# Kernel tuning notes

Hardware: AMD Instinct MI355X
Metric: run time of the kernel (lower is better)

## Reference

```python
import jax, jax.numpy as jnp
import numpy as np

N = 100000
E = 1600000
IN_FEATS = 256
HID = 128


def _graph_conv(x, W, b, src, dst, n_nodes):
    # DGL GraphConv with norm='both':
    #   out = D_in^{-1/2} * A * (D_out^{-1/2} * x @ W) + b
    ones = jnp.ones(src.shape[0], dtype=x.dtype)
    deg_out = jax.ops.segment_sum(ones, src, num_segments=n_nodes)
    deg_in = jax.ops.segment_sum(ones, dst, num_segments=n_nodes)
    norm_src = jnp.maximum(deg_out, 1.0) ** -0.5  # [N]
    norm_dst = jnp.maximum(deg_in, 1.0) ** -0.5   # [N]
    h = (x * norm_src[:, None]) @ W               # [N, HID]
    msg = h[src]                                  # [E, HID] gather
    agg = jax.ops.segment_sum(msg, dst, num_segments=n_nodes)  # [N, HID] scatter-add
    return agg * norm_dst[:, None] + b


def setup_inputs() -> dict:
    key = jax.random.key(0)
    ks = jax.random.split(key, 12)
    x = jax.random.normal(ks[0], (N, IN_FEATS), dtype=jnp.float32)
    src0 = jax.random.randint(ks[1], (E,), 0, N, dtype=jnp.int32)
    dst0 = jax.random.randint(ks[2], (E,), 0, N, dtype=jnp.int32)
    src1 = jax.random.randint(ks[3], (E,), 0, N, dtype=jnp.int32)
    dst1 = jax.random.randint(ks[4], (E,), 0, N, dtype=jnp.int32)
    s_e = 1.0 / np.sqrt(IN_FEATS)
    s_h = 1.0 / np.sqrt(HID)
    We = jax.random.uniform(ks[5], (IN_FEATS, HID), jnp.float32, -s_e, s_e)
    be = jax.random.uniform(ks[6], (HID,), jnp.float32, -s_e, s_e)
    W1 = jax.random.uniform(ks[7], (HID, HID), jnp.float32, -s_h, s_h)
    b1 = jnp.zeros((HID,), jnp.float32)
    W2 = jax.random.uniform(ks[8], (HID, HID), jnp.float32, -s_h, s_h)
    b2 = jnp.zeros((HID,), jnp.float32)
    return {"x": x, "We": We, "be": be, "W1": W1, "b1": b1, "W2": W2, "b2": b2,
            "src0": src0, "dst0": dst0, "src1": src1, "dst1": dst1}


def reference(x, We, be, W1, b1, W2, b2, src0, dst0, src1, dst1):
    n = x.shape[0]
    h = x @ We + be                                   # embed
    h = jax.nn.relu(_graph_conv(h, W1, b1, src0, dst0, n))
    h = jax.nn.relu(_graph_conv(h, W2, b2, src1, dst1, n))
    return h
```

## Files before the change

kernel.cpp:

```cpp
#include <hip/hip_runtime.h>

#define HID 128
#define NBUCK 512
#define BSHIFT 8
#define NB 512
#define M4 (4 * NBUCK * NB)
#define STAGE_CAP 8192
#define PCAP 7168

typedef __attribute__((ext_vector_type(8))) short bf16x8;
typedef __attribute__((ext_vector_type(4))) float f32x4;

__device__ __forceinline__ unsigned short f2bf(float f) {
    union { float f; unsigned u; } v; v.f = f;
    unsigned r = v.u + 0x7fff + ((v.u >> 16) & 1);
    return (unsigned short)(r >> 16);
}
__device__ __forceinline__ float bf2f(unsigned short b) {
    union { float f; unsigned u; } v; v.u = ((unsigned)b) << 16;
    return v.f;
}

__device__ __forceinline__ void gload_lds16(const void* g, void* l) {
    __builtin_amdgcn_global_load_lds(
        (const __attribute__((address_space(1))) void*)g,
        (__attribute__((address_space(3))) void*)l, 16, 0, 0);
}

__global__ __launch_bounds__(256) void bucket_count_all(
    const int* __restrict__ k0, const int* __restrict__ k1,
    const int* __restrict__ k2, const int* __restrict__ k3,
    int* __restrict__ counts, int E, int chunk) {
    __shared__ int h[4][NBUCK];
    int tid = threadIdx.x;
    #pragma unroll
    for (int j = 0; j < 8; ++j) ((int*)h)[tid + j * 256] = 0;
    __syncthreads();
    int base = blockIdx.x * chunk;
    int end = min(base + chunk, E);
    const int* keys[4] = {k0, k1, k2, k3};
    #pragma unroll
    for (int p = 0; p < 4; ++p) {
        const int* kp = keys[p];
        for (int i = base + tid; i < end; i += 256)
            atomicAdd(&h[p][kp[i] >> BSHIFT], 1);
    }
    __syncthreads();
    #pragma unroll
    for (int p = 0; p < 4; ++p) {
        counts[((p << 9) + tid) * NB + blockIdx.x] = h[p][tid];
        counts[((p << 9) + tid + 256) * NB + blockIdx.x] = h[p][tid + 256];
    }
}

__global__ __launch_bounds__(256) void scan_a(int* __restrict__ data, int* __restrict__ partials, int m) {
    __shared__ int sdata[256];
    int base = blockIdx.x * 1024;
    int tid = threadIdx.x;
    int v[4]; int s = 0;
    #pragma unroll
    for (int i = 0; i < 4; ++i) { int idx = base + tid * 4 + i; v[i] = (idx < m) ? data[idx] : 0; s += v[i]; }
    sdata[tid] = s; __syncthreads();
    for (int off = 1; off < 256; off <<= 1) {
        int t = (tid >= off) ? sdata[tid - off] : 0; __syncthreads();
        sdata[tid] += t; __syncthreads();
    }
    int excl = sdata[tid] - s;
    if (tid == 255) partials[blockIdx.x] = sdata[255];
    int run = excl;
    #pragma unroll
    for (int i = 0; i < 4; ++i) { int idx = base + tid * 4 + i; if (idx < m) data[idx] = run; run += v[i]; }
}

__global__ __launch_bounds__(1024) void scan_b(int* __restrict__ partials, int nb) {
    __shared__ int sdata[1024];
    int tid = threadIdx.x;
    int v = (tid < nb) ? partials[tid] : 0;
    sdata[tid] = v; __syncthreads();
    for (int off = 1; off < 1024; off <<= 1) {
        int t = (tid >= off) ? sdata[tid - off] : 0; __syncthreads();
        sdata[tid] += t; __syncthreads();
    }
    if (tid < nb) partials[tid] = sdata[tid] - v;
}

__global__ __launch_bounds__(256) void scan_c(int* __restrict__ data, const int* __restrict__ partials, int m) {
    int i = blockIdx.x * 256 + threadIdx.x;
    if (i < m) data[i] += partials[i >> 10];
}

__global__ __launch_bounds__(256) void bucket_scatter_all(
    const int* __restrict__ k0, const int* __restrict__ k1,
    const int* __restrict__ k2, const int* __restrict__ k3,
    const int* __restrict__ pay0, const int* __restrict__ pay1,
    const int* __restrict__ scanned, unsigned* __restrict__ bucketed,
    int E, int chunk) {
    __shared__ unsigned cur[4][NBUCK];
    int tid = threadIdx.x;
    int blk = blockIdx.x;
    #pragma unroll
    for (int p = 0; p < 4; ++p) {
        cur[p][tid]       = (unsigned)scanned[((p << 9) + tid) * NB + blk];
        cur[p][tid + 256] = (unsigned)scanned[((p << 9) + tid + 256) * NB + blk];
    }
    __syncthreads();
    int base = blk * chunk;
    int end = min(base + chunk, E);
    const int* keys[4] = {k0, k1, k2, k3};
    const int* pays[4] = {pay0, pay1, nullptr, nullptr};
    #pragma unroll
    for (int p = 0; p < 4; ++p) {
        const int* kp = keys[p];
        const int* pp = pays[p];
        for (int i = base + tid; i < end; i += 256) {
            int k = kp[i];
            int b = k >> BSHIFT;
            unsigned pay = pp ? (unsigned)pp[i] : 0u;
            unsigned pos = atomicAdd(&cur[p][b], 1u);
            bucketed[pos] = ((unsigned)(k & 255) << 17) | pay;
        }
    }
}

__global__ __launch_bounds__(256) void bucket_finalize(
    const unsigned* __restrict__ bucketed, const int* __restrict__ scanned,
    int* __restrict__ prow0, int* __restrict__ prow1,
    int* __restrict__ din0, int* __restrict__ din1,
    int* __restrict__ dout0, int* __restrict__ dout1,
    int* __restrict__ csr0, int* __restrict__ csr1, int n, int E) {
    __shared__ unsigned stage[STAGE_CAP];
    __shared__ int cnt[256];
    __shared__ int sd[256];
    __shared__ int pexcl[256];
    __shared__ int cur[256];
    int tid = threadIdx.x;
    int g = blockIdx.x;
    int p = g >> 9;
    int b = g & 511;
    int start = scanned[g * NB];
    int end = (g == 4 * NBUCK - 1) ? 4 * E : scanned[(g + 1) * NB];
    if (end - start > STAGE_CAP) end = start + STAGE_CAP;
    int len = end - start;
    int node0 = b << BSHIFT;

    cnt[tid] = 0;
    __syncthreads();
    if (p < 2) {
        for (int i = tid; i < len; i += 256) {
            unsigned v = bucketed[start + i];
            stage[i] = v;
            atomicAdd(&cnt[v >> 17], 1);
        }
    } else {
        for (int i = tid; i < len; i += 256)
            atomicAdd(&cnt[bucketed[start + i] >> 17], 1);
    }
    __syncthreads();

    if (p >= 2) {
        int* dout = (p == 2) ? dout0 : dout1;
        int node = node0 + tid;
        if (node < n) dout[node] = cnt[tid];
        return;
    }

    int c = cnt[tid];
    int pc = (c + 15) & ~15;
    sd[tid] = pc;
    __syncthreads();
    for (int off = 1; off < 256; off <<= 1) {
        int t = (tid >= off) ? sd[tid - off] : 0; __syncthreads();
        sd[tid] += t; __syncthreads();
    }
    pexcl[tid] = sd[tid] - pc;
    cur[tid] = 0;
    __syncthreads();
    int ptot = sd[255];
    if (ptot > PCAP) ptot = PCAP;

    int* csr  = (p == 0) ? csr0  : csr1;
    int* prow = (p == 0) ? prow0 : prow1;
    int* din  = (p == 0) ? din0  : din1;
    int node = node0 + tid;
    if (node < n) { prow[node] = b * PCAP + pexcl[tid]; din[node] = c; }

    const int base = b * PCAP;
    for (int j = tid; j < ptot; j += 256) csr[base + j] = n;
    __syncthreads();
    for (int i = tid; i < len; i += 256) {
        unsigned w = stage[i];
        int nl = (int)(w >> 17);
        int pos = base + pexcl[nl] + atomicAdd(&cur[nl], 1);
        csr[pos] = (int)(w & 0x1FFFFu);
    }
}

__device__ __forceinline__ size_t bswz_idx(int k, int col) {
    int s = k >> 5, lh = (k >> 3) & 3, j = k & 7;
    int c = col >> 4, lc = col & 15;
    return ((((size_t)s * 8 + c) * 64 + (lh * 16 + lc)) * 8 + j);
}

__global__ __launch_bounds__(256) void weight_fuse(
    const float* __restrict__ We, const float* __restrict__ be,
    const float* __restrict__ W1,
    unsigned short* __restrict__ B1h, unsigned short* __restrict__ B1l,
    float* __restrict__ cv) {
    __shared__ float w1[128][128];
    int tid = threadIdx.x;
    #pragma unroll
    for (int it = 0; it < 16; ++it) {
        int s = tid + it * 256;
        int r = s >> 5, c4 = (s & 31) << 2;
        *(float4*)&w1[r][c4] = *(const float4*)&W1[r * 128 + c4];
    }
    __syncthreads();
    int j = tid & 127;
    int half = tid >> 7;
    if (blockIdx.x == 128) {
        if (half) return;
        float sum = 0.f;
        for (int k = 0; k < 128; ++k) sum += be[k] * w1[k][j];
        cv[j] = sum;
        return;
    }
    int i = blockIdx.x * 2 + half;
    const float* arow = &We[i * 128];
    float sum = 0.f;
    for (int k = 0; k < 128; ++k) sum += arow[k] * w1[k][j];
    unsigned short h = f2bf(sum);
    unsigned short l = f2bf(sum - bf2f(h));
    size_t o = bswz_idx(i, j);
    B1h[o] = h; B1l[o] = l;
}

__global__ __launch_bounds__(256) void swizzle_split(
    const float* __restrict__ W, unsigned short* __restrict__ Bh,
    unsigned short* __restrict__ Bl, int K) {
    int idx = blockIdx.x * 256 + threadIdx.x;
    if (idx >= K * 128) return;
    int k = idx >> 7, col = idx & 127;
    float v = W[idx];
    unsigned short h = f2bf(v);
    unsigned short l = f2bf(v - bf2f(h));
    size_t o = bswz_idx(k, col);
    Bh[o] = h; Bl[o] = l;
}

template <int K, bool AFP32>
__global__ __launch_bounds__(512) void gemm_lds(
    const void* __restrict__ X_,
    const unsigned short* __restrict__ Bh, const unsigned short* __restrict__ Bl,
    const float* __restrict__ cvec, const int* __restrict__ degs,
    unsigned short* __restrict__ T, int n) {
    constexpr int NS = K / 32;
    __shared__ __align__(16) char smem[2 * 16384];
    const int tid = threadIdx.x;
    const int wave = tid >> 6;
    const int lane = tid & 63;
    const int lr = lane & 15;
    const int lk = lane >> 4;
    const int row0 = blockIdx.x * 128 + wave * 16;
    const int grow = row0 + lr;
    const bool vr = grow < n;

    f32x4 acc[8];
    #pragma unroll
    for (int c = 0; c < 8; ++c) acc[c] = (f32x4)0.f;

    auto stage_slab = [&](int s, char* dst) {
        #pragma unroll
        for (int it = 0; it < 2; ++it) {
            int u = tid + it * 512;
            int f = u >> 6;
            int c = f >> 1, plane = f & 1;
            const unsigned short* srcArr = plane ? Bl : Bh;
            const char* g = (const char*)srcArr +
                ((size_t)(s * 512 + c * 64 + (u & 63)) * 16);
            gload_lds16(g, dst + u * 16);
        }
    };

    stage_slab(0, smem);

    const float* pxf = AFP32 ? (const float*)X_ + (size_t)grow * K + lk * 8 : nullptr;
    const unsigned short* pxb = AFP32 ? nullptr : (const unsigned short*)X_ + (size_t)grow * K + lk * 8;
    float4 a0 = make_float4(0.f, 0.f, 0.f, 0.f), a1 = a0;
    bf16x8 ab = (bf16x8)0;
    if (AFP32) {
        if (vr) { a0 = *(const float4*)pxf; a1 = *(const float4*)(pxf + 4); }
    } else {
        if (vr) ab = *(const bf16x8*)pxb;
    }

    #pragma unroll
    for (int s = 0; s < NS; ++s) {
        __syncthreads();
        if (s + 1 < NS) stage_slab(s + 1, smem + ((s + 1) & 1) * 16384);

        float4 n0 = make_float4(0.f, 0.f, 0.f, 0.f), n1 = n0;
        bf16x8 nb = (bf16x8)0;
        if (s + 1 < NS && vr) {
            if (AFP32) {
                n0 = *(const float4*)(pxf + (s + 1) * 32);
                n1 = *(const float4*)(pxf + (s + 1) * 32 + 4);
            } else {
                nb = *(const bf16x8*)(pxb + (s + 1) * 32);
            }
        }

        bf16x8 ah, al;
        if (AFP32) {
            float av[8] = {a0.x, a0.y, a0.z, a0.w, a1.x, a1.y, a1.z, a1.w};
            #pragma unroll
            for (int j = 0; j < 8; ++j) {
                unsigned short h = f2bf(av[j]);
                ah[j] = (short)h;
                al[j] = (short)f2bf(av[j] - bf2f(h));
            }
        } else {
            ah = ab;
        }

        const char* base = smem + (s & 1) * 16384 + lane * 16;
        #pragma unroll
        for (int c = 0; c < 8; ++c) {
            bf16x8 bh = *(const bf16x8*)(base + (c * 2) * 1024);
            bf16x8 bl = *(const bf16x8*)(base + (c * 2 + 1) * 1024);
            acc[c] = __builtin_amdgcn_mfma_f32_16x16x32_bf16(ah, bh, acc[c], 0, 0, 0);
            acc[c] = __builtin_amdgcn_mfma_f32_16x16x32_bf16(ah, bl, acc[c], 0, 0, 0);
            if (AFP32)
                acc[c] = __builtin_amdgcn_mfma_f32_16x16x32_bf16(al, bh, acc[c], 0, 0, 0);
        }
        a0 = n0; a1 = n1; ab = nb;
    }

    #pragma unroll
    for (int r = 0; r < 4; ++r) {
        int orow = row0 + lk * 4 + r;
        if (orow >= n) continue;
        float norm = rsqrtf(fmaxf((float)degs[orow], 1.0f));
        #pragma unroll
        for (int c = 0; c < 8; ++c) {
            float v = acc[c][r];
            if (cvec) v += cvec[c * 16 + lr];
            T[(size_t)orow * 128 + c * 16 + lr] = f2bf(v * norm);
        }
    }
}

template <bool OUT_BF16>
__global__ __launch_bounds__(256) void aggregate(
    const unsigned short* __restrict__ T, const int* __restrict__ prow,
    const int* __restrict__ din, const int* __restrict__ csr,
    const float* __restrict__ bias, void* __restrict__ out_, int n) {
    const int wave = threadIdx.x >> 6;
    const int lane = threadIdx.x & 63;
    const int half = lane >> 5;
    const int l32 = lane & 31;
    const int node = blockIdx.x * 4 + wave;
    if (node >= n) return;
    const int beg = prow[node];
    const int d = din[node];
    const int plen = (d + 15) & ~15;
    float a0 = 0.f, a1 = 0.f, a2 = 0.f, a3 = 0.f;
    for (int e = beg; e < beg + plen; e += 16) {
        int sidx[8];
        #pragma unroll
        for (int j = 0; j < 8; ++j) sidx[j] = csr[e + j * 2 + half];
        #pragma unroll
        for (int j = 0; j < 8; ++j) {
            uint2 u = *(const uint2*)&T[(size_t)sidx[j] * 128 + l32 * 4];
            a0 += __uint_as_float(u.x << 16);
            a1 += __uint_as_float(u.x & 0xffff0000u);
            a2 += __uint_as_float(u.y << 16);
            a3 += __uint_as_float(u.y & 0xffff0000u);
        }
    }
    a0 += __shfl_xor(a0, 32);
    a1 += __shfl_xor(a1, 32);
    a2 += __shfl_xor(a2, 32);
    a3 += __shfl_xor(a3, 32);
    if (half == 0) {
        float norm = rsqrtf(fmaxf((float)d, 1.0f));
        float4 bv = *(const float4*)&bias[l32 * 4];
        float o0 = fmaxf(a0 * norm + bv.x, 0.f);
        float o1 = fmaxf(a1 * norm + bv.y, 0.f);
        float o2 = fmaxf(a2 * norm + bv.z, 0.f);
        float o3 = fmaxf(a3 * norm + bv.w, 0.f);
        if (OUT_BF16) {
            unsigned w0 = (unsigned)f2bf(o0) | ((unsigned)f2bf(o1) << 16);
            unsigned w1 = (unsigned)f2bf(o2) | ((unsigned)f2bf(o3) << 16);
            uint2* dst = (uint2*)((unsigned short*)out_ + (size_t)node * 128 + l32 * 4);
            *dst = make_uint2(w0, w1);
        } else {
            float4* dst = (float4*)((float*)out_ + (size_t)node * 128 + l32 * 4);
            *dst = make_float4(o0, o1, o2, o3);
        }
    }
}

extern "C" void kernel_launch(void* const* d_in, const int* in_sizes, int n_in,
                              void* d_out, int out_size, void* d_ws, size_t ws_size,
                              hipStream_t stream) {
    const float* x   = (const float*)d_in[0];
    const float* We  = (const float*)d_in[1];
    const float* be  = (const float*)d_in[2];
    const float* W1  = (const float*)d_in[3];
    const float* b1  = (const float*)d_in[4];
    const float* W2  = (const float*)d_in[5];
    const float* b2  = (const float*)d_in[6];
    const int* src0  = (const int*)d_in[7];
    const int* dst0  = (const int*)d_in[8];
    const int* src1  = (const int*)d_in[9];
    const int* dst1  = (const int*)d_in[10];
    float* out = (float*)d_out;

    const int n = in_sizes[0] / 256;
    const int E = in_sizes[7];
    const int chunk = (E + NB - 1) / NB;

    char* p = (char*)d_ws;
    auto carve = [&](size_t bytes) -> void* {
        void* r = (void*)p;
        p += (bytes + 511) & ~(size_t)511;
        return r;
    };
    unsigned short* t        = (unsigned short*)carve(((size_t)n + 1) * HID * 2);
    unsigned*       bucketed = (unsigned*)carve((size_t)4 * E * 4);
    int*            counts   = (int*)carve((size_t)M4 * 4);
    int*            partials = (int*)carve(1024 * 4);
    int*            csr0     = (int*)carve((size_t)NBUCK * PCAP * 4);
    int*            csr1     = (int*)carve((size_t)NBUCK * PCAP * 4);
    int*            prow0    = (int*)carve((size_t)n * 4);
    int*            prow1    = (int*)carve((size_t)n * 4);
    int*            din0     = (int*)carve((size_t)n * 4);
    int*            din1     = (int*)carve((size_t)n * 4);
    int*            dout0    = (int*)carve((size_t)n * 4);
    int*            dout1    = (int*)carve((size_t)n * 4);
    unsigned short* B1h      = (unsigned short*)carve(256 * HID * 2);
    unsigned short* B1l      = (unsigned short*)carve(256 * HID * 2);
    unsigned short* B2h      = (unsigned short*)carve(128 * HID * 2);
    unsigned short* B2l      = (unsigned short*)carve(128 * HID * 2);
    float*          cv       = (float*)carve(HID * 4);

    unsigned short* h1 = (unsigned short*)bucketed;

    const int gGemm  = (n + 127) / 128;
    const int gAggN  = (n + 3) / 4;
    const int gScanA = (M4 + 1023) / 1024;
    const int gScanC = (M4 + 255) / 256;

    hipMemsetAsync(t + (size_t)n * HID, 0, HID * 2, stream);

    bucket_count_all<<<NB, 256, 0, stream>>>(dst0, dst1, src0, src1, counts, E, chunk);
    scan_a<<<gScanA, 256, 0, stream>>>(counts, partials, M4);
    scan_b<<<1, 1024, 0, stream>>>(partials, gScanA);
    scan_c<<<gScanC, 256, 0, stream>>>(counts, partials, M4);
    bucket_scatter_all<<<NB, 256, 0, stream>>>(dst0, dst1, src0, src1, src0, src1,
                                               counts, bucketed, E, chunk);
    bucket_finalize<<<4 * NBUCK, 256, 0, stream>>>(bucketed, counts, prow0, prow1,
                                                   din0, din1, dout0, dout1, csr0, csr1, n, E);

    weight_fuse<<<129, 256, 0, stream>>>(We, be, W1, B1h, B1l, cv);
    swizzle_split<<<(128 * 128 + 255) / 256, 256, 0, stream>>>(W2, B2h, B2l, 128);

    gemm_lds<256, true><<<gGemm, 512, 0, stream>>>((const void*)x, B1h, B1l, cv, dout0, t, n);
    aggregate<true><<<gAggN, 256, 0, stream>>>(t, prow0, din0, csr0, b1, (void*)h1, n);
    gemm_lds<128, false><<<gGemm, 512, 0, stream>>>((const void*)h1, B2h, B2l, nullptr, dout1, t, n);
    aggregate<false><<<gAggN, 256, 0, stream>>>(t, prow1, din1, csr1, b2, (void*)out, n);
}
```

Measured before the change: 306.7 us.

## Hold weight slices in registers in persistent GEMM, fold scan fixup into consumers

The GEMM now keeps each wave's 16-column slice of the split-bf16 weights in registers for the whole kernel. It runs as a persistent grid of 1024 blocks that loop over 16-row tiles, replacing the double-buffered LDS staging. Each wave in a block now reads the same 16 rows of A, so A loads are repeated eight times per block, relying on cache reuse. Separately, the scan_c pass is removed by adding the block partials directly where the scanned offsets are read, and the two weight-prep kernels are merged into one launch.

Measured after the change: 405.8 us. 1.32x slower.

```diff
diff --git a/kernel.cpp b/kernel.cpp
--- a/kernel.cpp
+++ b/kernel.cpp
@@ -21,12 +21,6 @@
     return v.f;
 }
 
-__device__ __forceinline__ void gload_lds16(const void* g, void* l) {
-    __builtin_amdgcn_global_load_lds(
-        (const __attribute__((address_space(1))) void*)g,
-        (__attribute__((address_space(3))) void*)l, 16, 0, 0);
-}
-
 __global__ __launch_bounds__(256) void bucket_count_all(
     const int* __restrict__ k0, const int* __restrict__ k1,
     const int* __restrict__ k2, const int* __restrict__ k3,
@@ -84,24 +78,21 @@
     if (tid < nb) partials[tid] = sdata[tid] - v;
 }
 
-__global__ __launch_bounds__(256) void scan_c(int* __restrict__ data, const int* __restrict__ partials, int m) {
-    int i = blockIdx.x * 256 + threadIdx.x;
-    if (i < m) data[i] += partials[i >> 10];
-}
-
 __global__ __launch_bounds__(256) void bucket_scatter_all(
     const int* __restrict__ k0, const int* __restrict__ k1,
     const int* __restrict__ k2, const int* __restrict__ k3,
     const int* __restrict__ pay0, const int* __restrict__ pay1,
-    const int* __restrict__ scanned, unsigned* __restrict__ bucketed,
-    int E, int chunk) {
+    const int* __restrict__ scanned, const int* __restrict__ partials,
+    unsigned* __restrict__ bucketed, int E, int chunk) {
     __shared__ unsigned cur[4][NBUCK];
     int tid = threadIdx.x;
     int blk = blockIdx.x;
     #pragma unroll
     for (int p = 0; p < 4; ++p) {
-        cur[p][tid]       = (unsigned)scanned[((p << 9) + tid) * NB + blk];
-        cur[p][tid + 256] = (unsigned)scanned[((p << 9) + tid + 256) * NB + blk];
+        int i0 = ((p << 9) + tid) * NB + blk;
+        int i1 = ((p << 9) + tid + 256) * NB + blk;
+        cur[p][tid]       = (unsigned)(scanned[i0] + partials[i0 >> 10]);
+        cur[p][tid + 256] = (unsigned)(scanned[i1] + partials[i1 >> 10]);
     }
     __syncthreads();
     int base = blk * chunk;
@@ -124,6 +115,7 @@
 
 __global__ __launch_bounds__(256) void bucket_finalize(
     const unsigned* __restrict__ bucketed, const int* __restrict__ scanned,
+    const int* __restrict__ partials,
     int* __restrict__ prow0, int* __restrict__ prow1,
     int* __restrict__ din0, int* __restrict__ din1,
     int* __restrict__ dout0, int* __restrict__ dout1,
@@ -137,8 +129,11 @@
     int g = blockIdx.x;
     int p = g >> 9;
     int b = g & 511;
-    int start = scanned[g * NB];
-    int end = (g == 4 * NBUCK - 1) ? 4 * E : scanned[(g + 1) * NB];
+    int i0 = g * NB;
+    int start = scanned[i0] + partials[i0 >> 10];
+    int end;
+    if (g == 4 * NBUCK - 1) end = 4 * E;
+    else { int i1 = (g + 1) * NB; end = scanned[i1] + partials[i1 >> 10]; }
     if (end - start > STAGE_CAP) end = start + STAGE_CAP;
     int len = end - start;
     int node0 = b << BSHIFT;
@@ -201,13 +196,25 @@
     return ((((size_t)s * 8 + c) * 64 + (lh * 16 + lc)) * 8 + j);
 }
 
-__global__ __launch_bounds__(256) void weight_fuse(
+__global__ __launch_bounds__(256) void weight_prep(
     const float* __restrict__ We, const float* __restrict__ be,
-    const float* __restrict__ W1,
+    const float* __restrict__ W1, const float* __restrict__ W2,
     unsigned short* __restrict__ B1h, unsigned short* __restrict__ B1l,
+    unsigned short* __restrict__ B2h, unsigned short* __restrict__ B2l,
     float* __restrict__ cv) {
+    int tid = threadIdx.x;
+    if (blockIdx.x >= 129) {
+        int idx = (blockIdx.x - 129) * 256 + tid;
+        if (idx >= 128 * 128) return;
+        int k = idx >> 7, col = idx & 127;
+        float v = W2[idx];
+        unsigned short h = f2bf(v);
+        unsigned short l = f2bf(v - bf2f(h));
+        size_t o = bswz_idx(k, col);
+        B2h[o] = h; B2l[o] = l;
+        return;
+    }
     __shared__ float w1[128][128];
-    int tid = threadIdx.x;
     #pragma unroll
     for (int it = 0; it < 16; ++it) {
         int s = tid + it * 256;
@@ -234,115 +241,83 @@
     B1h[o] = h; B1l[o] = l;
 }
 
-__global__ __launch_bounds__(256) void swizzle_split(
-    const float* __restrict__ W, unsigned short* __restrict__ Bh,
-    unsigned short* __restrict__ Bl, int K) {
-    int idx = blockIdx.x * 256 + threadIdx.x;
-    if (idx >= K * 128) return;
-    int k = idx >> 7, col = idx & 127;
-    float v = W[idx];
-    unsigned short h = f2bf(v);
-    unsigned short l = f2bf(v - bf2f(h));
-    size_t o = bswz_idx(k, col);
-    Bh[o] = h; Bl[o] = l;
-}
-
 template <int K, bool AFP32>
-__global__ __launch_bounds__(512) void gemm_lds(
+__global__ __launch_bounds__(512) void gemm_breg(
     const void* __restrict__ X_,
     const unsigned short* __restrict__ Bh, const unsigned short* __restrict__ Bl,
     const float* __restrict__ cvec, const int* __restrict__ degs,
     unsigned short* __restrict__ T, int n) {
     constexpr int NS = K / 32;
-    __shared__ __align__(16) char smem[2 * 16384];
     const int tid = threadIdx.x;
     const int wave = tid >> 6;
     const int lane = tid & 63;
     const int lr = lane & 15;
     const int lk = lane >> 4;
-    const int row0 = blockIdx.x * 128 + wave * 16;
-    const int grow = row0 + lr;
-    const bool vr = grow < n;
-
-    f32x4 acc[8];
-    #pragma unroll
-    for (int c = 0; c < 8; ++c) acc[c] = (f32x4)0.f;
-
-    auto stage_slab = [&](int s, char* dst) {
+    const int c = wave;
+
+    const bf16x8* pBh = (const bf16x8*)Bh;
+    const bf16x8* pBl = (const bf16x8*)Bl;
+    bf16x8 rbh[NS], rbl[NS];
+    #pragma unroll
+    for (int s = 0; s < NS; ++s) {
+        rbh[s] = pBh[s * 512 + c * 64 + lane];
+        rbl[s] = pBl[s * 512 + c * 64 + lane];
+    }
+
+    const int tiles = (n + 15) >> 4;
+    for (int rt = blockIdx.x; rt < tiles; rt += gridDim.x) {
+        const int row0 = rt << 4;
+        const int grow = row0 + lr;
+        const int growc = (grow < n) ? grow : (n - 1);
+        const float* pxf = (const float*)X_ + (size_t)growc * K + lk * 8;
+        const unsigned short* pxb = (const unsigned short*)X_ + (size_t)growc * K + lk * 8;
+
+        f32x4 acc = (f32x4)0.f;
+        float4 a0 = make_float4(0.f, 0.f, 0.f, 0.f), a1 = a0;
+        bf16x8 ab = (bf16x8)0;
+        if (AFP32) { a0 = *(const float4*)pxf; a1 = *(const float4*)(pxf + 4); }
+        else       { ab = *(const bf16x8*)pxb; }
+
         #pragma unroll
-        for (int it = 0; it < 2; ++it) {
-            int u = tid + it * 512;
-            int f = u >> 6;
-            int c = f >> 1, plane = f & 1;
-            const unsigned short* srcArr = plane ? Bl : Bh;
-            const char* g = (const char*)srcArr +
-                ((size_t)(s * 512 + c * 64 + (u & 63)) * 16);
-            gload_lds16(g, dst + u * 16);
-        }
-    };
-
-    stage_slab(0, smem);
-
-    const float* pxf = AFP32 ? (const float*)X_ + (size_t)grow * K + lk * 8 : nullptr;
-    const unsigned short* pxb = AFP32 ? nullptr : (const unsigned short*)X_ + (size_t)grow * K + lk * 8;
-    float4 a0 = make_float4(0.f, 0.f, 0.f, 0.f), a1 = a0;
-    bf16x8 ab = (bf16x8)0;
-    if (AFP32) {
-        if (vr) { a0 = *(const float4*)pxf; a1 = *(const float4*)(pxf + 4); }
-    } else {
-        if (vr) ab = *(const bf16x8*)pxb;
-    }
-
-    #pragma unroll
-    for (int s = 0; s < NS; ++s) {
-        __syncthreads();
-        if (s + 1 < NS) stage_slab(s + 1, smem + ((s + 1) & 1) * 16384);
-
-        float4 n0 = make_float4(0.f, 0.f, 0.f, 0.f), n1 = n0;
-        bf16x8 nb = (bf16x8)0;
-        if (s + 1 < NS && vr) {
+        for (int s = 0; s < NS; ++s) {
+            float4 n0 = make_float4(0.f, 0.f, 0.f, 0.f), n1 = n0;
+            bf16x8 nb = (bf16x8)0;
+            if (s + 1 < NS) {
+                if (AFP32) {
+                    n0 = *(const float4*)(pxf + (s + 1) * 32);
+                    n1 = *(const float4*)(pxf + (s + 1) * 32 + 4);
+                } else {
+                    nb = *(const bf16x8*)(pxb + (s + 1) * 32);
+                }
+            }
+
+            bf16x8 ah, al;
             if (AFP32) {
-                n0 = *(const float4*)(pxf + (s + 1) * 32);
-                n1 = *(const float4*)(pxf + (s + 1) * 32 + 4);
+                float av[8] = {a0.x, a0.y, a0.z, a0.w, a1.x, a1.y, a1.z, a1.w};
+                #pragma unroll
+                for (int j = 0; j < 8; ++j) {
+                    unsigned short h = f2bf(av[j]);
+                    ah[j] = (short)h;
+                    al[j] = (short)f2bf(av[j] - bf2f(h));
+                }
             } else {
-                nb = *(const bf16x8*)(pxb + (s + 1) * 32);
+                ah = ab;
             }
-        }
-
-        bf16x8 ah, al;
-        if (AFP32) {
-            float av[8] = {a0.x, a0.y, a0.z, a0.w, a1.x, a1.y, a1.z, a1.w};
-            #pragma unroll
-            for (int j = 0; j < 8; ++j) {
-                unsigned short h = f2bf(av[j]);
-                ah[j] = (short)h;
-                al[j] = (short)f2bf(av[j] - bf2f(h));
-            }
-        } else {
-            ah = ab;
-        }
-
-        const char* base = smem + (s & 1) * 16384 + lane * 16;
+
+            acc = __builtin_amdgcn_mfma_f32_16x16x32_bf16(ah, rbh[s], acc, 0, 0, 0);
+            acc = __builtin_amdgcn_mfma_f32_16x16x32_bf16(ah, rbl[s], acc, 0, 0, 0);
+            if (AFP32)
+                acc = __builtin_amdgcn_mfma_f32_16x16x32_bf16(al, rbh[s], acc, 0, 0, 0);
+
+            a0 = n0; a1 = n1; ab = nb;
+        }
+
         #pragma unroll
-        for (int c = 0; c < 8; ++c) {
-            bf16x8 bh = *(const bf16x8*)(base + (c * 2) * 1024);
-            bf16x8 bl = *(const bf16x8*)(base + (c * 2 + 1) * 1024);
-            acc[c] = __builtin_amdgcn_mfma_f32_16x16x32_bf16(ah, bh, acc[c], 0, 0, 0);
-            acc[c] = __builtin_amdgcn_mfma_f32_16x16x32_bf16(ah, bl, acc[c], 0, 0, 0);
-            if (AFP32)
-                acc[c] = __builtin_amdgcn_mfma_f32_16x16x32_bf16(al, bh, acc[c], 0, 0, 0);
-        }
-        a0 = n0; a1 = n1; ab = nb;
-    }
-
-    #pragma unroll
-    for (int r = 0; r < 4; ++r) {
-        int orow = row0 + lk * 4 + r;
-        if (orow >= n) continue;
-        float norm = rsqrtf(fmaxf((float)degs[orow], 1.0f));
-        #pragma unroll
-        for (int c = 0; c < 8; ++c) {
-            float v = acc[c][r];
+        for (int r = 0; r < 4; ++r) {
+            int orow = row0 + lk * 4 + r;
+            if (orow >= n) continue;
+            float norm = rsqrtf(fmaxf((float)degs[orow], 1.0f));
+            float v = acc[r];
             if (cvec) v += cvec[c * 16 + lr];
             T[(size_t)orow * 128 + c * 16 + lr] = f2bf(v * norm);
         }
@@ -446,27 +421,24 @@
 
     unsigned short* h1 = (unsigned short*)bucketed;
 
-    const int gGemm  = (n + 127) / 128;
+    const int gGemm  = 1024;
     const int gAggN  = (n + 3) / 4;
     const int gScanA = (M4 + 1023) / 1024;
-    const int gScanC = (M4 + 255) / 256;
 
     hipMemsetAsync(t + (size_t)n * HID, 0, HID * 2, stream);
 
     bucket_count_all<<<NB, 256, 0, stream>>>(dst0, dst1, src0, src1, counts, E, chunk);
     scan_a<<<gScanA, 256, 0, stream>>>(counts, partials, M4);
     scan_b<<<1, 1024, 0, stream>>>(partials, gScanA);
-    scan_c<<<gScanC, 256, 0, stream>>>(counts, partials, M4);
     bucket_scatter_all<<<NB, 256, 0, stream>>>(dst0, dst1, src0, src1, src0, src1,
-                                               counts, bucketed, E, chunk);
-    bucket_finalize<<<4 * NBUCK, 256, 0, stream>>>(bucketed, counts, prow0, prow1,
+                                               counts, partials, bucketed, E, chunk);
+    bucket_finalize<<<4 * NBUCK, 256, 0, stream>>>(bucketed, counts, partials, prow0, prow1,
                                                    din0, din1, dout0, dout1, csr0, csr1, n, E);
 
-    weight_fuse<<<129, 256, 0, stream>>>(We, be, W1, B1h, B1l, cv);
-    swizzle_split<<<(128 * 128 + 255) / 256, 256, 0, stream>>>(W2, B2h, B2l, 128);
-
-    gemm_lds<256, true><<<gGemm, 512, 0, stream>>>((const void*)x, B1h, B1l, cv, dout0, t, n);
+    weight_prep<<<193, 256, 0, stream>>>(We, be, W1, W2, B1h, B1l, B2h, B2l, cv);
+
+    gemm_breg<256, true><<<gGemm, 512, 0, stream>>>((const void*)x, B1h, B1l, cv, dout0, t, n);
     aggregate<true><<<gAggN, 256, 0, stream>>>(t, prow0, din0, csr0, b1, (void*)h1, n);
-    gemm_lds<128, false><<<gGemm, 512, 0, stream>>>((const void*)h1, B2h, B2l, nullptr, dout1, t, n);
+    gemm_breg<128, false><<<gGemm, 512, 0, stream>>>((const void*)h1, B2h, B2l, nullptr, dout1, t, n);
     aggregate<false><<<gAggN, 256, 0, stream>>>(t, prow1, din1, csr1, b2, (void*)out, n);
 }
```
